# Kernel optimization log

Hardware: AMD Instinct MI355X
Metric: run time of the kernel (lower is better)

Reference implementation:

```python
import jax, jax.numpy as jnp
import numpy as np

N_NODES = 50000
N_REL = 5
N_BASES = 5
OUT = 300
N_EDGES = 800000


def setup_inputs() -> dict:
    key = jax.random.key(0)
    ks = jax.random.split(key, 6)
    edge_index = jax.random.randint(ks[0], (2, N_EDGES), 0, N_NODES)
    edge_type = jax.random.randint(ks[1], (N_EDGES,), 0, N_REL)
    edge_norm = jax.random.normal(ks[2], (N_EDGES,), dtype=jnp.float32)
    # Learned params of RGCNConv(in=N_NODES, out=OUT, R=5, num_bases=5)
    basis = jax.random.normal(ks[3], (N_BASES, N_NODES, OUT), dtype=jnp.float32) * 0.02
    comp = jax.random.normal(ks[4], (N_REL, N_BASES), dtype=jnp.float32)
    root = jax.random.normal(ks[5], (N_NODES, OUT), dtype=jnp.float32) * 0.02
    bias = jnp.zeros((OUT,), dtype=jnp.float32)
    return dict(edge_index=edge_index, edge_type=edge_type, edge_norm=edge_norm,
                basis=basis, comp=comp, root=root, bias=bias)


def reference(edge_index, edge_type, edge_norm, basis, comp, root, bias):
    src, dst = edge_index[0], edge_index[1]
    # Basis decomposition: weight[r] = sum_b comp[r,b] * basis[b]  -> [R, N, OUT]
    weight = jnp.einsum('rb,bnd->rnd', comp, basis)
    # x=None => one-hot node features: per-edge message = weight[edge_type_e, src_e]
    msg = weight[edge_type, src]                                  # [E, OUT]
    # mean aggregation at destination (PyG RGCNConv default aggr='mean')
    agg = jax.ops.segment_sum(msg, dst, num_segments=N_NODES)     # [N, OUT]
    cnt = jax.ops.segment_sum(jnp.ones((msg.shape[0],), msg.dtype), dst,
                              num_segments=N_NODES)
    agg = agg / jnp.maximum(cnt, 1.0)[:, None]
    # root weight for one-hot x is a plain per-node row add, plus bias
    h = agg + root + bias
    return jax.nn.log_softmax(jax.nn.relu(h), axis=1)
```

## Files before the change

kernel.cpp:

```cpp
#include <hip/hip_runtime.h>
#include <hip/hip_bf16.h>
#include <hip/hip_fp16.h>
#include <string.h>

#define N_NODES 50000
#define N_REL 5
#define N_BASES 5
#define OUT 300
#define N_EDGES 800000
#define NBLK 196
#define BCAP 128

typedef float f4v __attribute__((ext_vector_type(4)));

__device__ __forceinline__ unsigned enc1(float x) {
    unsigned u = (unsigned)__half_as_ushort((__half)(x * 0.00390625f));
    unsigned s   = (u >> 15) & 1u;
    unsigned mag = u & 0x7fffu;
    unsigned m8  = (mag + 63u + ((mag >> 7) & 1u)) >> 7;
    return (s << 7) | m8;
}
__device__ __forceinline__ unsigned wenc(float x0, float x1, float x2, float x3) {
    return enc1(x0) | (enc1(x1) << 8) | (enc1(x2) << 16) | (enc1(x3) << 24);
}
__device__ __forceinline__ float2 dec2(unsigned v) {
    unsigned h = ((v & 0x80u)   << 8)  | ((v & 0x7fu)   << 7)
               | ((v & 0x8000u) << 16) | ((v & 0x7f00u) << 15);
    __half2 hh;
    memcpy(&hh, &h, 4);
    return __half22float2(hh);
}
__device__ __forceinline__ void wdec(unsigned w, float& x0, float& x1,
                                     float& x2, float& x3) {
    float2 lo = dec2(w);
    float2 hi = dec2(w >> 16);
    x0 = lo.x; x1 = lo.y; x2 = hi.x; x3 = hi.y;
}

__global__ void rgcn_zero(int* __restrict__ p, int n)
{
    int i = blockIdx.x * blockDim.x + threadIdx.x;
    if (i < n) p[i] = 0;
}

__global__ void rgcn_scatter_build(const float* __restrict__ basis,
                                   const float* __restrict__ comp,
                                   const int* __restrict__ srcA,
                                   const int* __restrict__ dstA,
                                   const int* __restrict__ typeA,
                                   int* __restrict__ cnt,
                                   int* __restrict__ bucket,
                                   unsigned* __restrict__ Wm,
                                   unsigned* __restrict__ Wt)
{
    const int gid = blockIdx.x * blockDim.x + threadIdx.x;
    const int gsz = gridDim.x * blockDim.x;

    for (int e = gid; e < N_EDGES; e += gsz) {
        const int d = dstA[e];
        const int pos = atomicAdd(&cnt[d], 1);
        if (pos < BCAP)
            bucket[d * BCAP + pos] = srcA[e] | (typeA[e] << 16);
    }

    float c[N_REL][N_BASES];
    #pragma unroll
    for (int t = 0; t < N_REL; ++t)
        #pragma unroll
        for (int b = 0; b < N_BASES; ++b)
            c[t][b] = comp[t * N_BASES + b];

    const int totm = N_NODES * 64;
    const int tota = totm + N_NODES * 11;
    for (int id = gid; id < tota; id += gsz) {
        size_t eoff;
        if (id < totm) {
            eoff = (size_t)(id >> 6) * OUT + 4 * (id & 63);
        } else {
            const int tid = id - totm;
            const int n = tid / 11;
            eoff = (size_t)n * OUT + 256 + 4 * (tid - n * 11);
        }
        f4v f[N_BASES];
        #pragma unroll
        for (int b = 0; b < N_BASES; ++b)
            f[b] = __builtin_nontemporal_load(
                (const f4v*)&basis[(size_t)b * N_NODES * OUT + eoff]);
        #pragma unroll
        for (int t = 0; t < N_REL; ++t) {
            float x0 = 0.f, x1 = 0.f, x2 = 0.f, x3 = 0.f;
            #pragma unroll
            for (int b = 0; b < N_BASES; ++b) {
                x0 += c[t][b] * f[b].x; x1 += c[t][b] * f[b].y;
                x2 += c[t][b] * f[b].z; x3 += c[t][b] * f[b].w;
            }
            const unsigned w = wenc(x0, x1, x2, x3);
            if (id < totm) Wm[(size_t)t * N_NODES * 64 + id] = w;
            else           Wt[(size_t)t * N_NODES * 11 + (id - totm)] = w;
        }
    }
}

__global__ __launch_bounds__(256) void rgcn_aggregate(
    const int* __restrict__ cnt, const int* __restrict__ bucket,
    const unsigned* __restrict__ Wm, const unsigned* __restrict__ Wt,
    const float* __restrict__ root, const float* __restrict__ bias,
    float* __restrict__ out)
{
    __shared__ float smrow[4][304];
    const int lane = (int)(threadIdx.x & 63);
    const int wid  = (int)(threadIdx.x >> 6);
    const int k    = lane & 15;
    const int g    = lane >> 4;
    const int node = blockIdx.x * 4 + wid;
    const int deg = cnt[node];
    const int s = node * BCAP;
    const int deg_c = min(deg, BCAP);
    const bool ktail = k < 11;
    const bool tail = lane < 11;

    const size_t ro = (size_t)node * OUT;
    const float4 rt0 = *(const float4*)&root[ro + 4 * lane];
    const float4 bi0 = *(const float4*)&bias[4 * lane];
    float4 rt1 = make_float4(0.f,0.f,0.f,0.f), bi1 = rt1;
    if (tail) {
        rt1 = *(const float4*)&root[ro + 256 + 4 * lane];
        bi1 = *(const float4*)&bias[256 + 4 * lane];
    }

    float a[16];
    #pragma unroll
    for (int j = 0; j < 16; ++j) a[j] = 0.f;
    float t0 = 0.f, t1 = 0.f, t2 = 0.f, t3 = 0.f;

    const int nb4 = (deg_c + 3) >> 2;
    if (deg_c <= 64) {
        const int clampL = (deg_c > 0) ? (deg_c - 1) : 0;
        const int pre = bucket[s + min(lane, clampL)];
        for (int bi = 0; bi < nb4; ++bi) {
            const int idx4 = (bi << 2) + g;
            const bool act = idx4 < deg_c;
            const int p = __shfl(pre, min(idx4, clampL), 64);
            const unsigned r = (unsigned)(p >> 16) * N_NODES + (p & 0xFFFF);
            const uint4 w = *(const uint4*)&Wm[r * 64u + 4u * (unsigned)k];
            unsigned wt = 0u;
            if (ktail) wt = Wt[r * 11u + (unsigned)k];
            if (act) {
                float x0, x1, x2, x3;
                wdec(w.x, x0,x1,x2,x3); a[0]+=x0;  a[1]+=x1;  a[2]+=x2;  a[3]+=x3;
                wdec(w.y, x0,x1,x2,x3); a[4]+=x0;  a[5]+=x1;  a[6]+=x2;  a[7]+=x3;
                wdec(w.z, x0,x1,x2,x3); a[8]+=x0;  a[9]+=x1;  a[10]+=x2; a[11]+=x3;
                wdec(w.w, x0,x1,x2,x3); a[12]+=x0; a[13]+=x1; a[14]+=x2; a[15]+=x3;
                wdec(wt,  x0,x1,x2,x3); t0+=x0;    t1+=x1;    t2+=x2;    t3+=x3;
            }
        }
    } else {
        const int e_end = s + deg_c;
        for (int bi = 0; bi < nb4; ++bi) {
            const int eidx = s + (bi << 2) + g;
            const bool act = eidx < e_end;
            const int p = bucket[act ? eidx : s];
            const unsigned r = (unsigned)(p >> 16) * N_NODES + (p & 0xFFFF);
            const uint4 w = *(const uint4*)&Wm[r * 64u + 4u * (unsigned)k];
            unsigned wt = 0u;
            if (ktail) wt = Wt[r * 11u + (unsigned)k];
            if (act) {
                float x0, x1, x2, x3;
                wdec(w.x, x0,x1,x2,x3); a[0]+=x0;  a[1]+=x1;  a[2]+=x2;  a[3]+=x3;
                wdec(w.y, x0,x1,x2,x3); a[4]+=x0;  a[5]+=x1;  a[6]+=x2;  a[7]+=x3;
                wdec(w.z, x0,x1,x2,x3); a[8]+=x0;  a[9]+=x1;  a[10]+=x2; a[11]+=x3;
                wdec(w.w, x0,x1,x2,x3); a[12]+=x0; a[13]+=x1; a[14]+=x2; a[15]+=x3;
                wdec(wt,  x0,x1,x2,x3); t0+=x0;    t1+=x1;    t2+=x2;    t3+=x3;
            }
        }
    }

    #pragma unroll
    for (int j = 0; j < 16; ++j) {
        a[j] += __shfl_down(a[j], 32, 64);
        a[j] += __shfl_down(a[j], 16, 64);
    }
    t0 += __shfl_down(t0, 32, 64); t1 += __shfl_down(t1, 32, 64);
    t2 += __shfl_down(t2, 32, 64); t3 += __shfl_down(t3, 32, 64);
    t0 += __shfl_down(t0, 16, 64); t1 += __shfl_down(t1, 16, 64);
    t2 += __shfl_down(t2, 16, 64); t3 += __shfl_down(t3, 16, 64);

    if (lane < 16) {
        #pragma unroll
        for (int q = 0; q < 4; ++q) {
            float4 f4 = make_float4(a[4*q+0], a[4*q+1], a[4*q+2], a[4*q+3]);
            *(float4*)&smrow[wid][16 * lane + 4 * q] = f4;
        }
    }
    if (lane < 11)
        *(float4*)&smrow[wid][256 + 4 * lane] = make_float4(t0, t1, t2, t3);
    __builtin_amdgcn_wave_barrier();

    const float4 aa = *(const float4*)&smrow[wid][4 * lane];
    float4 tt = make_float4(0.f, 0.f, 0.f, 0.f);
    if (tail) tt = *(const float4*)&smrow[wid][256 + 4 * lane];

    const float inv = 256.0f / fmaxf((float)deg, 1.0f);
    float v0 = fmaxf(aa.x * inv + rt0.x + bi0.x, 0.0f);
    float v1 = fmaxf(aa.y * inv + rt0.y + bi0.y, 0.0f);
    float v2 = fmaxf(aa.z * inv + rt0.z + bi0.z, 0.0f);
    float v3 = fmaxf(aa.w * inv + rt0.w + bi0.w, 0.0f);
    float v4 = 0.f, v5 = 0.f, v6 = 0.f, v7 = 0.f;
    if (tail) {
        v4 = fmaxf(tt.x * inv + rt1.x + bi1.x, 0.0f);
        v5 = fmaxf(tt.y * inv + rt1.y + bi1.y, 0.0f);
        v6 = fmaxf(tt.z * inv + rt1.z + bi1.z, 0.0f);
        v7 = fmaxf(tt.w * inv + rt1.w + bi1.w, 0.0f);
    }
    float m = fmaxf(fmaxf(fmaxf(v0, v1), fmaxf(v2, v3)),
                    fmaxf(fmaxf(v4, v5), fmaxf(v6, v7)));
    #pragma unroll
    for (int off = 32; off >= 1; off >>= 1) m = fmaxf(m, __shfl_xor(m, off, 64));
    float sum = __expf(v0 - m) + __expf(v1 - m) + __expf(v2 - m) + __expf(v3 - m);
    if (tail) sum += __expf(v4 - m) + __expf(v5 - m) + __expf(v6 - m) + __expf(v7 - m);
    #pragma unroll
    for (int off = 32; off >= 1; off >>= 1) sum += __shfl_xor(sum, off, 64);
    const float lse = m + logf(sum);
    *(float4*)&out[ro + 4 * lane] =
        make_float4(v0 - lse, v1 - lse, v2 - lse, v3 - lse);
    if (tail)
        *(float4*)&out[ro + 256 + 4 * lane] =
            make_float4(v4 - lse, v5 - lse, v6 - lse, v7 - lse);
}

__global__ void rgcn_edge_scatter(const int* __restrict__ edge_index,
                                  const int* __restrict__ edge_type,
                                  const float* __restrict__ basis,
                                  const float* __restrict__ comp,
                                  float* __restrict__ agg,
                                  float* __restrict__ cnt)
{
    const int lane = threadIdx.x & 63;
    const int wid  = (blockIdx.x * (blockDim.x >> 6)) + (threadIdx.x >> 6);
    const int nwav = gridDim.x * (blockDim.x >> 6);
    const int* __restrict__ src_arr = edge_index;
    const int* __restrict__ dst_arr = edge_index + N_EDGES;
    for (int e = wid; e < N_EDGES; e += nwav) {
        const int src = src_arr[e];
        const int dst = dst_arr[e];
        const int t   = edge_type[e];
        const float c0 = comp[t*N_BASES+0], c1 = comp[t*N_BASES+1],
                    c2 = comp[t*N_BASES+2], c3 = comp[t*N_BASES+3],
                    c4 = comp[t*N_BASES+4];
        const size_t rowoff = (size_t)src * OUT;
        const float* b0 = basis + rowoff;
        const float* b1 = basis + (size_t)1*N_NODES*OUT + rowoff;
        const float* b2 = basis + (size_t)2*N_NODES*OUT + rowoff;
        const float* b3 = basis + (size_t)3*N_NODES*OUT + rowoff;
        const float* b4 = basis + (size_t)4*N_NODES*OUT + rowoff;
        float* aout = agg + (size_t)dst * OUT;
        for (int d = lane; d < OUT; d += 64) {
            float m = c0*b0[d] + c1*b1[d] + c2*b2[d] + c3*b3[d] + c4*b4[d];
            atomicAdd(&aout[d], m);
        }
        if (lane == 0) atomicAdd(&cnt[dst], 1.0f);
    }
}

__global__ void rgcn_finalize(float* __restrict__ agg,
                              const float* __restrict__ cnt,
                              const float* __restrict__ root,
                              const float* __restrict__ bias)
{
    const int lane = threadIdx.x & 63;
    const int wid  = (blockIdx.x * (blockDim.x >> 6)) + (threadIdx.x >> 6);
    if (wid >= N_NODES) return;
    const size_t rowoff = (size_t)wid * OUT;
    const float inv = 1.0f / fmaxf(cnt[wid], 1.0f);
    float v[5];
    float lmax = 0.0f;
    #pragma unroll
    for (int kk = 0; kk < 5; ++kk) {
        int d = lane + kk * 64;
        if (d < OUT) {
            float h = agg[rowoff + d] * inv + root[rowoff + d] + bias[d];
            float r = fmaxf(h, 0.0f);
            v[kk] = r; lmax = fmaxf(lmax, r);
        } else v[kk] = 0.0f;
    }
    #pragma unroll
    for (int off = 32; off >= 1; off >>= 1) lmax = fmaxf(lmax, __shfl_xor(lmax, off, 64));
    float lsum = 0.0f;
    #pragma unroll
    for (int kk = 0; kk < 5; ++kk) { int d = lane + kk*64; if (d < OUT) lsum += __expf(v[kk]-lmax); }
    #pragma unroll
    for (int off = 32; off >= 1; off >>= 1) lsum += __shfl_xor(lsum, off, 64);
    const float lse = lmax + logf(lsum);
    #pragma unroll
    for (int kk = 0; kk < 5; ++kk) { int d = lane + kk*64; if (d < OUT) agg[rowoff+d] = v[kk]-lse; }
}

extern "C" void kernel_launch(void* const* d_in, const int* in_sizes, int n_in,
                              void* d_out, int out_size, void* d_ws, size_t ws_size,
                              hipStream_t stream) {
    const int*   edge_index = (const int*)d_in[0];
    const int*   edge_type  = (const int*)d_in[1];
    const float* basis      = (const float*)d_in[3];
    const float* comp       = (const float*)d_in[4];
    const float* root       = (const float*)d_in[5];
    const float* bias       = (const float*)d_in[6];

    const size_t o_cnt    = 0;
    const size_t o_bucket = 200192;
    const size_t o_Wm     = 25800192;
    const size_t o_Wt     = 89800192;
    const size_t need     = o_Wt + (size_t)N_REL * N_NODES * 11 * sizeof(unsigned);

    if (ws_size >= need) {
        int*      cnt    = (int*)((char*)d_ws + o_cnt);
        int*      bucket = (int*)((char*)d_ws + o_bucket);
        unsigned* Wm     = (unsigned*)((char*)d_ws + o_Wm);
        unsigned* Wt     = (unsigned*)((char*)d_ws + o_Wt);

        rgcn_zero<<<NBLK, 256, 0, stream>>>(cnt, N_NODES);
        rgcn_scatter_build<<<14649, 256, 0, stream>>>(basis, comp,
                                                      edge_index,
                                                      edge_index + N_EDGES,
                                                      edge_type,
                                                      cnt, bucket, Wm, Wt);
        rgcn_aggregate<<<(N_NODES + 3) / 4, 256, 0, stream>>>(
            cnt, bucket, Wm, Wt, root, bias, (float*)d_out);
    } else {
        float* agg = (float*)d_out;
        float* cnt = (float*)d_ws;
        hipMemsetAsync(agg, 0, (size_t)out_size * sizeof(float), stream);
        hipMemsetAsync(cnt, 0, (size_t)N_NODES * sizeof(float), stream);
        rgcn_edge_scatter<<<4096, 256, 0, stream>>>(edge_index, edge_type, basis,
                                                    comp, agg, cnt);
        const int blocks = (N_NODES + 3) / 4;
        rgcn_finalize<<<blocks, 256, 0, stream>>>(agg, cnt, root, bias);
    }
}
```

Before: 190.7 us.

## Simplify aggregate loop, defer root loads, and move edge scatter after weight build

The edge bucketing loop moves to the end of the build kernel, after the weight-combination pass. In the aggregate kernel, the two degree-dependent paths (a shuffle-broadcast prefetch of bucket entries for low degree, direct loads otherwise) merge into one path that loads bucket entries directly each iteration. Root and bias loads move from before the gather loop to just before their use. This lowers register pressure and code size, but adds a global load per iteration and exposes root-load latency that was previously hidden.

```diff
diff --git a/kernel.cpp b/kernel.cpp
--- a/kernel.cpp
+++ b/kernel.cpp
@@ -55,13 +55,6 @@
 {
     const int gid = blockIdx.x * blockDim.x + threadIdx.x;
     const int gsz = gridDim.x * blockDim.x;
-
-    for (int e = gid; e < N_EDGES; e += gsz) {
-        const int d = dstA[e];
-        const int pos = atomicAdd(&cnt[d], 1);
-        if (pos < BCAP)
-            bucket[d * BCAP + pos] = srcA[e] | (typeA[e] << 16);
-    }
 
     float c[N_REL][N_BASES];
     #pragma unroll
@@ -99,6 +92,13 @@
             else           Wt[(size_t)t * N_NODES * 11 + (id - totm)] = w;
         }
     }
+
+    for (int e = gid; e < N_EDGES; e += gsz) {
+        const int d = dstA[e];
+        const int pos = atomicAdd(&cnt[d], 1);
+        if (pos < BCAP)
+            bucket[d * BCAP + pos] = srcA[e] | (typeA[e] << 16);
+    }
 }
 
 __global__ __launch_bounds__(256) void rgcn_aggregate(
@@ -115,63 +115,30 @@
     const int node = blockIdx.x * 4 + wid;
     const int deg = cnt[node];
     const int s = node * BCAP;
-    const int deg_c = min(deg, BCAP);
+    const int e_end = s + min(deg, BCAP);
     const bool ktail = k < 11;
-    const bool tail = lane < 11;
-
-    const size_t ro = (size_t)node * OUT;
-    const float4 rt0 = *(const float4*)&root[ro + 4 * lane];
-    const float4 bi0 = *(const float4*)&bias[4 * lane];
-    float4 rt1 = make_float4(0.f,0.f,0.f,0.f), bi1 = rt1;
-    if (tail) {
-        rt1 = *(const float4*)&root[ro + 256 + 4 * lane];
-        bi1 = *(const float4*)&bias[256 + 4 * lane];
-    }
 
     float a[16];
     #pragma unroll
     for (int j = 0; j < 16; ++j) a[j] = 0.f;
     float t0 = 0.f, t1 = 0.f, t2 = 0.f, t3 = 0.f;
 
-    const int nb4 = (deg_c + 3) >> 2;
-    if (deg_c <= 64) {
-        const int clampL = (deg_c > 0) ? (deg_c - 1) : 0;
-        const int pre = bucket[s + min(lane, clampL)];
-        for (int bi = 0; bi < nb4; ++bi) {
-            const int idx4 = (bi << 2) + g;
-            const bool act = idx4 < deg_c;
-            const int p = __shfl(pre, min(idx4, clampL), 64);
-            const unsigned r = (unsigned)(p >> 16) * N_NODES + (p & 0xFFFF);
-            const uint4 w = *(const uint4*)&Wm[r * 64u + 4u * (unsigned)k];
-            unsigned wt = 0u;
-            if (ktail) wt = Wt[r * 11u + (unsigned)k];
-            if (act) {
-                float x0, x1, x2, x3;
-                wdec(w.x, x0,x1,x2,x3); a[0]+=x0;  a[1]+=x1;  a[2]+=x2;  a[3]+=x3;
-                wdec(w.y, x0,x1,x2,x3); a[4]+=x0;  a[5]+=x1;  a[6]+=x2;  a[7]+=x3;
-                wdec(w.z, x0,x1,x2,x3); a[8]+=x0;  a[9]+=x1;  a[10]+=x2; a[11]+=x3;
-                wdec(w.w, x0,x1,x2,x3); a[12]+=x0; a[13]+=x1; a[14]+=x2; a[15]+=x3;
-                wdec(wt,  x0,x1,x2,x3); t0+=x0;    t1+=x1;    t2+=x2;    t3+=x3;
-            }
-        }
-    } else {
-        const int e_end = s + deg_c;
-        for (int bi = 0; bi < nb4; ++bi) {
-            const int eidx = s + (bi << 2) + g;
-            const bool act = eidx < e_end;
-            const int p = bucket[act ? eidx : s];
-            const unsigned r = (unsigned)(p >> 16) * N_NODES + (p & 0xFFFF);
-            const uint4 w = *(const uint4*)&Wm[r * 64u + 4u * (unsigned)k];
-            unsigned wt = 0u;
-            if (ktail) wt = Wt[r * 11u + (unsigned)k];
-            if (act) {
-                float x0, x1, x2, x3;
-                wdec(w.x, x0,x1,x2,x3); a[0]+=x0;  a[1]+=x1;  a[2]+=x2;  a[3]+=x3;
-                wdec(w.y, x0,x1,x2,x3); a[4]+=x0;  a[5]+=x1;  a[6]+=x2;  a[7]+=x3;
-                wdec(w.z, x0,x1,x2,x3); a[8]+=x0;  a[9]+=x1;  a[10]+=x2; a[11]+=x3;
-                wdec(w.w, x0,x1,x2,x3); a[12]+=x0; a[13]+=x1; a[14]+=x2; a[15]+=x3;
-                wdec(wt,  x0,x1,x2,x3); t0+=x0;    t1+=x1;    t2+=x2;    t3+=x3;
-            }
+    const int nb4 = (min(deg, BCAP) + 3) >> 2;
+    for (int bi = 0; bi < nb4; ++bi) {
+        const int eidx = s + (bi << 2) + g;
+        const bool act = eidx < e_end;
+        const int p = bucket[act ? eidx : s];
+        const unsigned r = (unsigned)(p >> 16) * N_NODES + (p & 0xFFFF);
+        const uint4 w = *(const uint4*)&Wm[r * 64u + 4u * (unsigned)k];
+        unsigned wt = 0u;
+        if (ktail) wt = Wt[r * 11u + (unsigned)k];
+        if (act) {
+            float x0, x1, x2, x3;
+            wdec(w.x, x0,x1,x2,x3); a[0]+=x0;  a[1]+=x1;  a[2]+=x2;  a[3]+=x3;
+            wdec(w.y, x0,x1,x2,x3); a[4]+=x0;  a[5]+=x1;  a[6]+=x2;  a[7]+=x3;
+            wdec(w.z, x0,x1,x2,x3); a[8]+=x0;  a[9]+=x1;  a[10]+=x2; a[11]+=x3;
+            wdec(w.w, x0,x1,x2,x3); a[12]+=x0; a[13]+=x1; a[14]+=x2; a[15]+=x3;
+            wdec(wt,  x0,x1,x2,x3); t0+=x0;    t1+=x1;    t2+=x2;    t3+=x3;
         }
     }
 
@@ -197,16 +164,22 @@
     __builtin_amdgcn_wave_barrier();
 
     const float4 aa = *(const float4*)&smrow[wid][4 * lane];
+    const bool tail = lane < 11;
     float4 tt = make_float4(0.f, 0.f, 0.f, 0.f);
     if (tail) tt = *(const float4*)&smrow[wid][256 + 4 * lane];
 
     const float inv = 256.0f / fmaxf((float)deg, 1.0f);
+    const size_t ro = (size_t)node * OUT;
+    const float4 rt0 = *(const float4*)&root[ro + 4 * lane];
+    const float4 bi0 = *(const float4*)&bias[4 * lane];
     float v0 = fmaxf(aa.x * inv + rt0.x + bi0.x, 0.0f);
     float v1 = fmaxf(aa.y * inv + rt0.y + bi0.y, 0.0f);
     float v2 = fmaxf(aa.z * inv + rt0.z + bi0.z, 0.0f);
     float v3 = fmaxf(aa.w * inv + rt0.w + bi0.w, 0.0f);
     float v4 = 0.f, v5 = 0.f, v6 = 0.f, v7 = 0.f;
     if (tail) {
+        const float4 rt1 = *(const float4*)&root[ro + 256 + 4 * lane];
+        const float4 bi1 = *(const float4*)&bias[256 + 4 * lane];
         v4 = fmaxf(tt.x * inv + rt1.x + bi1.x, 0.0f);
         v5 = fmaxf(tt.y * inv + rt1.y + bi1.y, 0.0f);
         v6 = fmaxf(tt.z * inv + rt1.z + bi1.z, 0.0f);
```

Result: no change. 187.4 us (-1.7%).
